# Kernel optimization log

Measured on AMD Instinct MI355X. Metric: run time of the kernel, lower is better.

Reference implementation:

```python
import jax, jax.numpy as jnp
import numpy as np

# ---- static config (from init_kwargs) ----
B, H, W, C = 4, 256, 256, 96
WS, SS, NH = 8, 4, 3            # window_size, shift_size, num_heads
N = WS * WS                     # tokens per window = 64
NW = (H // WS) * (W // WS)      # windows per image = 1024
HD = C // NH                    # head_dim = 32
SCALE = HD ** -0.5
MLP_H = int(C * 4.0)
EPS = 1e-5


def _relative_position_index():
    coords = np.stack(np.meshgrid(np.arange(WS), np.arange(WS), indexing='ij'))  # (2, WS, WS)
    cf = coords.reshape(2, -1)                       # (2, N)
    rel = (cf[:, :, None] - cf[:, None, :]).transpose(1, 2, 0).astype(np.int64)  # (N, N, 2)
    rel[:, :, 0] += WS - 1
    rel[:, :, 1] += WS - 1
    rel[:, :, 0] *= 2 * WS - 1
    return rel.sum(-1)                               # (N, N) in [0, (2WS-1)^2)


def _attn_mask():
    img = np.zeros((H, W))
    cnt = 0
    slices = (slice(0, -WS), slice(-WS, -SS), slice(-SS, None))
    for hs in slices:
        for ws in slices:
            img[hs, ws] = cnt
            cnt += 1
    m = img.reshape(H // WS, WS, W // WS, WS).transpose(0, 2, 1, 3).reshape(-1, N)  # (NW, N)
    am = m[:, None, :] - m[:, :, None]               # (NW, N, N)
    return np.where(am != 0, -100.0, 0.0).astype(np.float32)


def setup_inputs() -> dict:
    key = jax.random.key(0)
    ks = jax.random.split(key, 8)
    std = 0.02
    inp = {
        'x': jax.random.normal(ks[0], (B, H * W, C), jnp.float32),
        'g1': jnp.ones((C,), jnp.float32),
        'b1': jnp.zeros((C,), jnp.float32),
        'qkv_w': jax.random.normal(ks[1], (3 * C, C), jnp.float32) * std,
        'qkv_b': jnp.zeros((3 * C,), jnp.float32),
        'rpb_table': jax.random.normal(ks[2], ((2 * WS - 1) ** 2, NH), jnp.float32) * std,
        'proj_w': jax.random.normal(ks[3], (C, C), jnp.float32) * std,
        'proj_b': jnp.zeros((C,), jnp.float32),
        'g2': jnp.ones((C,), jnp.float32),
        'b2': jnp.zeros((C,), jnp.float32),
        'fc1_w': jax.random.normal(ks[4], (MLP_H, C), jnp.float32) * std,
        'fc1_b': jnp.zeros((MLP_H,), jnp.float32),
        'fc2_w': jax.random.normal(ks[5], (C, MLP_H), jnp.float32) * std,
        'fc2_b': jnp.zeros((C,), jnp.float32),
        'attn_mask': jnp.asarray(_attn_mask()),
        'rel_index': jnp.asarray(_relative_position_index(), jnp.int32),
    }
    return inp


def _ln(x, g, b):
    mu = jnp.mean(x, -1, keepdims=True)
    var = jnp.mean(jnp.square(x - mu), -1, keepdims=True)
    return (x - mu) * jax.lax.rsqrt(var + EPS) * g + b


def reference(x, g1, b1, qkv_w, qkv_b, rpb_table, proj_w, proj_b,
              g2, b2, fc1_w, fc1_b, fc2_w, fc2_b, attn_mask, rel_index):
    shortcut = x
    h = _ln(x, g1, b1).reshape(B, H, W, C)
    # cyclic shift
    h = jnp.roll(h, (-SS, -SS), axis=(1, 2))
    # window partition -> (B*NW, N, C)
    xw = h.reshape(B, H // WS, WS, W // WS, WS, C).transpose(0, 1, 3, 2, 4, 5).reshape(-1, N, C)
    # qkv projection
    qkv = (xw @ qkv_w.T + qkv_b).reshape(-1, N, 3, NH, HD).transpose(2, 0, 3, 1, 4)  # (3, B_, NH, N, HD)
    q, k, v = qkv[0] * SCALE, qkv[1], qkv[2]
    attn = jnp.einsum('bhnd,bhmd->bhnm', q, k)       # (B_, NH, N, N)
    # gathered relative position bias: (N, N, NH) -> (NH, N, N)
    bias = rpb_table[rel_index].transpose(2, 0, 1)
    attn = attn + bias[None]
    # shifted-window mask
    attn = attn.reshape(B, NW, NH, N, N) + attn_mask[None, :, None]
    attn = jax.nn.softmax(attn.reshape(-1, NH, N, N), axis=-1)
    o = jnp.einsum('bhnm,bhmd->bhnd', attn, v).transpose(0, 2, 1, 3).reshape(-1, N, C)
    o = o @ proj_w.T + proj_b
    # window reverse + reverse shift
    o = o.reshape(B, H // WS, W // WS, WS, WS, C).transpose(0, 1, 3, 2, 4, 5).reshape(B, H, W, C)
    o = jnp.roll(o, (SS, SS), axis=(1, 2)).reshape(B, H * W, C)
    x = shortcut + o
    h2 = _ln(x, g2, b2)
    h2 = jax.nn.gelu(h2 @ fc1_w.T + fc1_b, approximate=False) @ fc2_w.T + fc2_b
    return x + h2
```

## Files before the change

kernel.cpp:

```cpp
#include <hip/hip_runtime.h>
#include <hip/hip_bf16.h>
#include <math.h>

constexpr float SCALE_ = 0.17677669529663687f;

typedef float f32x4 __attribute__((ext_vector_type(4)));
typedef short bf16x8 __attribute__((ext_vector_type(8)));
typedef short short4v __attribute__((ext_vector_type(4)));
#define MFMA __builtin_amdgcn_mfma_f32_16x16x32_bf16


__device__ inline short f2bf(float f) {
    __hip_bfloat16 h = __float2bfloat16(f);
    return *reinterpret_cast<short*>(&h);
}
__device__ inline float bf2f(short s) {
    union { unsigned u; float f; } v; v.u = ((unsigned)(unsigned short)s) << 16;
    return v.f;
}
__device__ inline float gelu_erf(float v) {
    float z  = v * 0.70710678f;
    float z2 = fminf(z * z, 1.5f);
    float p  =      0.00012055333f;
    p = p * z2 -    0.00085483270f;
    p = p * z2 +    0.0052239776f;
    p = p * z2 -    0.0268661706f;
    p = p * z2 +    0.1128379167f;
    p = p * z2 -    0.3761263890f;
    p = p * z2 +    1.1283791671f;
    float er = z * p;
    float t  = 0.5f * v;
    return t * er + t;
}

__global__ __launch_bounds__(256)
void prep_weights(const float* __restrict__ qkv_w, const float* __restrict__ proj_w,
                  const float* __restrict__ fc1_w, const float* __restrict__ fc2_w,
                  short* __restrict__ ws)
{
    int i = blockIdx.x * 256 + threadIdx.x;
    if (i >= 110592) return;
    float v;
    if      (i < 27648)  v = qkv_w[i];
    else if (i < 36864)  v = proj_w[i - 27648];
    else if (i < 73728)  v = fc1_w[i - 36864];
    else                 v = fc2_w[i - 73728];
    ws[i] = f2bf(v);
}

__global__ __launch_bounds__(256)
void prep_comb(const float* __restrict__ rpb, const int* __restrict__ rel,
               const float* __restrict__ mask, short* __restrict__ comb)
{
    int e = blockIdx.x * 256 + threadIdx.x;
    if (e >= 49152) return;
    int t   = e / 12288;
    int rem = e - t * 12288;
    int h   = rem >> 12;
    int ij  = rem & 4095;
    const int rep[4] = {0, 31, 992, 1023};
    comb[e] = f2bf(rpb[rel[ij] * 3 + h] + mask[(long)rep[t] * 4096 + ij]);
}

__global__ __launch_bounds__(256, 3)
void attn_kernel(const float* __restrict__ x,
                 const float* __restrict__ g1, const float* __restrict__ b1,
                 const short* __restrict__ qkv_wb, const float* __restrict__ qkv_b,
                 const short* __restrict__ proj_wb, const float* __restrict__ proj_b,
                 const short* __restrict__ comb,
                 float* __restrict__ xnew)
{
    __shared__ short aL[64][104];
    __shared__ short qpL[64][104];
    __shared__ short kL[64][104];
    __shared__ short vT[96][72];

    const int tid  = threadIdx.x;
    const int wave = tid >> 6, lane = tid & 63;
    const int lr = lane & 15, lg = lane >> 4;
    const int blk = blockIdx.x;
    const int b = blk >> 10, wi = blk & 1023;
    const int wh = wi >> 5, ww = wi & 31;
    const int mtyp = ((wh == 31) ? 2 : 0) + ((ww == 31) ? 1 : 0);

    auto tok_of = [&](int n) -> int {
        int r = n >> 3, c = n & 7;
        int gh = (wh * 8 + r + 4) & 255;
        int gw = (ww * 8 + c + 4) & 255;
        return b * 65536 + gh * 256 + gw;
    };

    {
        const int n = tid >> 2, s = tid & 3;
        const float* xr = x + (long)tok_of(n) * 96 + s * 24;
        float xv[24];
        #pragma unroll
        for (int i = 0; i < 6; i++) {
            float4 t = ((const float4*)xr)[i];
            xv[4*i]=t.x; xv[4*i+1]=t.y; xv[4*i+2]=t.z; xv[4*i+3]=t.w;
        }
        float s1 = 0.f, s2 = 0.f;
        #pragma unroll
        for (int i = 0; i < 24; i++) { s1 += xv[i]; s2 += xv[i]*xv[i]; }
        s1 += __shfl_xor(s1, 1); s2 += __shfl_xor(s2, 1);
        s1 += __shfl_xor(s1, 2); s2 += __shfl_xor(s2, 2);
        float mu = s1 * (1.0f/96.0f);
        float var = s2 * (1.0f/96.0f) - mu*mu;
        float rs = rsqrtf(var + 1e-5f);
        #pragma unroll
        for (int c = 0; c < 24; c++)
            aL[n][s*24+c] = f2bf((xv[c]-mu)*rs*g1[s*24+c] + b1[s*24+c]);
    }
    __syncthreads();

    {
        const int wm = wave >> 1, wn = wave & 1;
        bf16x8 afr[2][3];
        #pragma unroll
        for (int mt = 0; mt < 2; mt++)
            #pragma unroll
            for (int kt = 0; kt < 3; kt++)
                afr[mt][kt] = *(const bf16x8*)&aL[(2*wm+mt)*16 + lr][kt*32 + lg*8];
        for (int nt0 = 0; nt0 < 9; nt0++) {
            const int nt = wn * 9 + nt0;
            const int o  = nt * 16 + lr;
            bf16x8 bfr[3];
            #pragma unroll
            for (int kt = 0; kt < 3; kt++)
                bfr[kt] = *(const bf16x8*)&qkv_wb[(long)o * 96 + kt*32 + lg*8];
            const float bias = qkv_b[o];
            #pragma unroll
            for (int mt = 0; mt < 2; mt++) {
                f32x4 acc = {bias, bias, bias, bias};
                #pragma unroll
                for (int kt = 0; kt < 3; kt++)
                    acc = MFMA(afr[mt][kt], bfr[kt], acc, 0, 0, 0);
                const int row0 = (2*wm+mt)*16 + lg*4;
                if (nt < 6) {
                    #pragma unroll
                    for (int r = 0; r < 4; r++) qpL[row0+r][o] = f2bf(acc[r]*SCALE_);
                } else if (nt < 12) {
                    #pragma unroll
                    for (int r = 0; r < 4; r++) kL[row0+r][o-96] = f2bf(acc[r]);
                } else {
                    #pragma unroll
                    for (int r = 0; r < 4; r++) vT[o-192][row0+r] = f2bf(acc[r]);
                }
            }
        }
    }
    __syncthreads();

    bf16x8 qf[3];
    #pragma unroll
    for (int h = 0; h < 3; h++)
        qf[h] = *(const bf16x8*)&qpL[wave*16 + lr][h*32 + lg*8];

    for (int h = 0; h < 3; h++) {
        const short* cb = comb + (mtyp * 3 + h) * 4096;
        float sv[4][4];
        #pragma unroll
        for (int nt = 0; nt < 4; nt++) {
            bf16x8 kf = *(const bf16x8*)&kL[nt*16 + lr][h*32 + lg*8];
            f32x4 s = MFMA(qf[h], kf, (f32x4){0.f,0.f,0.f,0.f}, 0, 0, 0);
            #pragma unroll
            for (int r = 0; r < 4; r++) {
                int i = wave*16 + lg*4 + r;
                int j = nt*16 + lr;
                sv[nt][r] = s[r] + bf2f(cb[i*64 + j]);
            }
        }
        float mx[4], sm[4];
        #pragma unroll
        for (int r = 0; r < 4; r++) {
            mx[r] = fmaxf(fmaxf(sv[0][r], sv[1][r]), fmaxf(sv[2][r], sv[3][r]));
            mx[r] = fmaxf(mx[r], __shfl_xor(mx[r], 1));
            mx[r] = fmaxf(mx[r], __shfl_xor(mx[r], 2));
            mx[r] = fmaxf(mx[r], __shfl_xor(mx[r], 4));
            mx[r] = fmaxf(mx[r], __shfl_xor(mx[r], 8));
            sm[r] = 0.f;
        }
        #pragma unroll
        for (int nt = 0; nt < 4; nt++)
            #pragma unroll
            for (int r = 0; r < 4; r++) { sv[nt][r] = __expf(sv[nt][r]-mx[r]); sm[r] += sv[nt][r]; }
        #pragma unroll
        for (int r = 0; r < 4; r++) {
            sm[r] += __shfl_xor(sm[r], 1);
            sm[r] += __shfl_xor(sm[r], 2);
            sm[r] += __shfl_xor(sm[r], 4);
            sm[r] += __shfl_xor(sm[r], 8);
            sm[r] = 1.0f / sm[r];
        }
        #pragma unroll
        for (int nt = 0; nt < 4; nt++)
            #pragma unroll
            for (int r = 0; r < 4; r++)
                qpL[wave*16 + lg*4 + r][nt*16 + lr] = f2bf(sv[nt][r]*sm[r]);

        bf16x8 pf[2];
        #pragma unroll
        for (int kt = 0; kt < 2; kt++)
            pf[kt] = *(const bf16x8*)&qpL[wave*16 + lr][kt*32 + lg*8];
        #pragma unroll
        for (int nt = 0; nt < 2; nt++) {
            f32x4 acc = {0.f,0.f,0.f,0.f};
            #pragma unroll
            for (int kt = 0; kt < 2; kt++) {
                bf16x8 vf = *(const bf16x8*)&vT[h*32 + nt*16 + lr][kt*32 + lg*8];
                acc = MFMA(pf[kt], vf, acc, 0, 0, 0);
            }
            #pragma unroll
            for (int r = 0; r < 4; r++)
                aL[wave*16 + lg*4 + r][h*32 + nt*16 + lr] = f2bf(acc[r]);
        }
    }
    __syncthreads();

    {
        const int wm = wave >> 1, wn = wave & 1;
        bf16x8 afr[2][3];
        #pragma unroll
        for (int mt = 0; mt < 2; mt++)
            #pragma unroll
            for (int kt = 0; kt < 3; kt++)
                afr[mt][kt] = *(const bf16x8*)&aL[(2*wm+mt)*16 + lr][kt*32 + lg*8];
        for (int nt0 = 0; nt0 < 3; nt0++) {
            const int nt = wn * 3 + nt0;
            const int c  = nt * 16 + lr;
            bf16x8 bfr[3];
            #pragma unroll
            for (int kt = 0; kt < 3; kt++)
                bfr[kt] = *(const bf16x8*)&proj_wb[(long)c * 96 + kt*32 + lg*8];
            const float bias = proj_b[c];
            #pragma unroll
            for (int mt = 0; mt < 2; mt++) {
                f32x4 acc = {bias, bias, bias, bias};
                #pragma unroll
                for (int kt = 0; kt < 3; kt++)
                    acc = MFMA(afr[mt][kt], bfr[kt], acc, 0, 0, 0);
                #pragma unroll
                for (int r = 0; r < 4; r++) {
                    int i = (2*wm+mt)*16 + lg*4 + r;
                    long ad = (long)tok_of(i) * 96 + c;
                    xnew[ad] = acc[r] + x[ad];
                }
            }
        }
    }
}

__global__ __launch_bounds__(256, 4)
void mlp_kernel(const float* __restrict__ g2, const float* __restrict__ b2,
                const short* __restrict__ fc1_wb, const float* __restrict__ fc1_b,
                const short* __restrict__ fc2_wb, const float* __restrict__ fc2_b,
                float* __restrict__ xio)
{
    __shared__ short smem[4 * 3328];
    const int tid  = threadIdx.x;
    const int wave = tid >> 6, lane = tid & 63;
    const int lr = lane & 15, lg = lane >> 4;
    short* wl = smem + wave * 3328;
    const long tok0 = (long)blockIdx.x * 128 + wave * 32;
    const long base = tok0 * 96;

    #pragma unroll
    for (int p = 0; p < 2; p++) {
        const int tl = p*16 + (lane >> 2);
        const int s  = lane & 3;
        const float* xr = xio + base + (long)tl * 96 + s * 24;
        float xv[24];
        #pragma unroll
        for (int i = 0; i < 6; i++) {
            float4 t = ((const float4*)xr)[i];
            xv[4*i]=t.x; xv[4*i+1]=t.y; xv[4*i+2]=t.z; xv[4*i+3]=t.w;
        }
        float s1 = 0.f, s2 = 0.f;
        #pragma unroll
        for (int i = 0; i < 24; i++) { s1 += xv[i]; s2 += xv[i]*xv[i]; }
        s1 += __shfl_xor(s1, 1); s2 += __shfl_xor(s2, 1);
        s1 += __shfl_xor(s1, 2); s2 += __shfl_xor(s2, 2);
        float mu  = s1 * (1.0f/96.0f);
        float var = s2 * (1.0f/96.0f) - mu*mu;
        float rs  = rsqrtf(var + 1e-5f);
        #pragma unroll
        for (int j = 0; j < 12; j++) {
            const int ch = s*24 + 2*j;
            unsigned lo = (unsigned short)f2bf((xv[2*j  ]-mu)*rs*g2[ch  ] + b2[ch  ]);
            unsigned hi = (unsigned short)f2bf((xv[2*j+1]-mu)*rs*g2[ch+1] + b2[ch+1]);
            *(unsigned*)&wl[tl*104 + ch] = lo | (hi << 16);
        }
    }
    bf16x8 bx[2][3];
    #pragma unroll
    for (int tt = 0; tt < 2; tt++)
        #pragma unroll
        for (int kt = 0; kt < 3; kt++)
            bx[tt][kt] = *(const bf16x8*)&wl[(tt*16+lr)*104 + kt*32 + lg*8];
    asm volatile("s_waitcnt lgkmcnt(0)" ::: "memory");

    f32x4 facc[2][6];
    #pragma unroll
    for (int nt = 0; nt < 6; nt++) {
        const float4 bb = *(const float4*)&fc2_b[nt*16 + lg*4];
        facc[0][nt] = (f32x4){bb.x, bb.y, bb.z, bb.w};
        facc[1][nt] = facc[0][nt];
    }

    for (int c = 0; c < 6; c++) {
        #pragma unroll
        for (int ss = 0; ss < 2; ss++) {
            f32x4 a1[2][2];
            #pragma unroll
            for (int h2 = 0; h2 < 2; h2++) {
                const int ht = ss*2 + h2;
                const int o  = c*64 + ht*16 + lr;
                bf16x8 wfr[3];
                #pragma unroll
                for (int kt = 0; kt < 3; kt++)
                    wfr[kt] = *(const bf16x8*)&fc1_wb[(long)o * 96 + kt*32 + lg*8];
                const float4 bi = *(const float4*)&fc1_b[c*64 + ht*16 + lg*4];
                const f32x4 binit = {bi.x, bi.y, bi.z, bi.w};
                #pragma unroll
                for (int tt = 0; tt < 2; tt++) {
                    f32x4 acc = binit;
                    #pragma unroll
                    for (int kt = 0; kt < 3; kt++)
                        acc = MFMA(wfr[kt], bx[tt][kt], acc, 0, 0, 0);
                    a1[h2][tt] = acc;
                }
            }
            #pragma unroll
            for (int h2 = 0; h2 < 2; h2++)
                #pragma unroll
                for (int tt = 0; tt < 2; tt++) {
                    short4v sv;
                    #pragma unroll
                    for (int r = 0; r < 4; r++)
                        sv[r] = f2bf(gelu_erf(a1[h2][tt][r]));
                    const int tok = tt*16 + lr;
                    const int hid = (ss*2 + h2)*16 + lg*4;
                    *(short4v*)&wl[tok*72 + hid] = sv;
                }
        }
        asm volatile("" ::: "memory");
        #pragma unroll
        for (int tt = 0; tt < 2; tt++) {
            bf16x8 hf[2];
            #pragma unroll
            for (int kt = 0; kt < 2; kt++)
                hf[kt] = *(const bf16x8*)&wl[(tt*16+lr)*72 + kt*32 + lg*8];
            #pragma unroll
            for (int nt = 0; nt < 6; nt++) {
                #pragma unroll
                for (int kt = 0; kt < 2; kt++) {
                    bf16x8 wf2 = *(const bf16x8*)&fc2_wb[(long)(nt*16+lr)*384 + c*64 + kt*32 + lg*8];
                    facc[tt][nt] = MFMA(wf2, hf[kt], facc[tt][nt], 0, 0, 0);
                }
            }
        }
        asm volatile("" ::: "memory");
    }

    #pragma unroll
    for (int tt = 0; tt < 2; tt++)
        #pragma unroll
        for (int nt = 0; nt < 6; nt++) {
            const long ad = base + (long)(tt*16 + lr) * 96 + nt*16 + lg*4;
            float4 o = *(const float4*)&xio[ad];
            o.x += facc[tt][nt][0]; o.y += facc[tt][nt][1];
            o.z += facc[tt][nt][2]; o.w += facc[tt][nt][3];
            *(float4*)&xio[ad] = o;
        }
}

extern "C" void kernel_launch(void* const* d_in, const int* in_sizes, int n_in,
                              void* d_out, int out_size, void* d_ws, size_t ws_size,
                              hipStream_t stream)
{
    const float* x      = (const float*)d_in[0];
    const float* g1     = (const float*)d_in[1];
    const float* b1     = (const float*)d_in[2];
    const float* qkv_w  = (const float*)d_in[3];
    const float* qkv_b  = (const float*)d_in[4];
    const float* rpb    = (const float*)d_in[5];
    const float* proj_w = (const float*)d_in[6];
    const float* proj_b = (const float*)d_in[7];
    const float* g2     = (const float*)d_in[8];
    const float* b2     = (const float*)d_in[9];
    const float* fc1_w  = (const float*)d_in[10];
    const float* fc1_b  = (const float*)d_in[11];
    const float* fc2_w  = (const float*)d_in[12];
    const float* fc2_b  = (const float*)d_in[13];
    const float* mask   = (const float*)d_in[14];
    const int*   rel    = (const int*)d_in[15];
    float* out = (float*)d_out;

    short* wsS    = (short*)d_ws;
    short* qkv_wb = wsS;
    short* proj_wb= wsS + 27648;
    short* fc1_wb = wsS + 36864;
    short* fc2_wb = wsS + 73728;
    short* comb   = wsS + 110592;

    prep_weights<<<432, 256, 0, stream>>>(qkv_w, proj_w, fc1_w, fc2_w, wsS);
    prep_comb<<<192, 256, 0, stream>>>(rpb, rel, mask, comb);
    attn_kernel<<<4096, 256, 0, stream>>>(x, g1, b1, qkv_wb, qkv_b,
                                          proj_wb, proj_b, comb, out);
    mlp_kernel<<<2048, 256, 0, stream>>>(g2, b2, fc1_wb, fc1_b, fc2_wb, fc2_b, out);
}
```

Baseline: 277.3 us.

## Split MLP tile across waves in 2x2 grid with shared hidden buffer

Before, each wave ran the full MLP on its own 32 tokens, so every wave streamed all fc1/fc2 weight rows. Now a 256-thread block handles 64 tokens, and its four waves form a 2x2 grid. Each wave computes half the hidden units for half the tokens in fc1, and half the output columns in fc2. The GELU hidden chunk goes to double-buffered shared memory and is shared across waves, which halves per-wave weight-fragment loads. The cost is block-wide __syncthreads each chunk and a doubled grid size.

```diff
diff --git a/kernel.cpp b/kernel.cpp
--- a/kernel.cpp
+++ b/kernel.cpp
@@ -256,19 +256,19 @@
                 const short* __restrict__ fc2_wb, const float* __restrict__ fc2_b,
                 float* __restrict__ xio)
 {
-    __shared__ short smem[4 * 3328];
+    __shared__ short smem[9216];
+    short (*aL)[104]    = (short(*)[104])smem;
+    short (*hch)[64][72] = (short(*)[64][72])smem;
+
     const int tid  = threadIdx.x;
     const int wave = tid >> 6, lane = tid & 63;
     const int lr = lane & 15, lg = lane >> 4;
-    short* wl = smem + wave * 3328;
-    const long tok0 = (long)blockIdx.x * 128 + wave * 32;
-    const long base = tok0 * 96;
-
-    #pragma unroll
-    for (int p = 0; p < 2; p++) {
-        const int tl = p*16 + (lane >> 2);
-        const int s  = lane & 3;
-        const float* xr = xio + base + (long)tl * 96 + s * 24;
+    const int wm = wave >> 1, wn = wave & 1;
+    const long base = (long)blockIdx.x * 6144;
+
+    {
+        const int n = tid >> 2, s = tid & 3;
+        const float* xr = xio + base + n * 96 + s * 24;
         float xv[24];
         #pragma unroll
         for (int i = 0; i < 6; i++) {
@@ -288,88 +288,89 @@
             const int ch = s*24 + 2*j;
             unsigned lo = (unsigned short)f2bf((xv[2*j  ]-mu)*rs*g2[ch  ] + b2[ch  ]);
             unsigned hi = (unsigned short)f2bf((xv[2*j+1]-mu)*rs*g2[ch+1] + b2[ch+1]);
-            *(unsigned*)&wl[tl*104 + ch] = lo | (hi << 16);
-        }
-    }
+            *(unsigned*)&aL[n][ch] = lo | (hi << 16);
+        }
+    }
+    __syncthreads();
+
     bf16x8 bx[2][3];
     #pragma unroll
     for (int tt = 0; tt < 2; tt++)
         #pragma unroll
         for (int kt = 0; kt < 3; kt++)
-            bx[tt][kt] = *(const bf16x8*)&wl[(tt*16+lr)*104 + kt*32 + lg*8];
-    asm volatile("s_waitcnt lgkmcnt(0)" ::: "memory");
-
-    f32x4 facc[2][6];
+            bx[tt][kt] = *(const bf16x8*)&aL[(wn*2+tt)*16 + lr][kt*32 + lg*8];
+    __syncthreads();
+
+    f32x4 facc[3][2];
     #pragma unroll
-    for (int nt = 0; nt < 6; nt++) {
-        const float4 bb = *(const float4*)&fc2_b[nt*16 + lg*4];
-        facc[0][nt] = (f32x4){bb.x, bb.y, bb.z, bb.w};
-        facc[1][nt] = facc[0][nt];
+    for (int nt = 0; nt < 3; nt++) {
+        const float4 bb = *(const float4*)&fc2_b[(wm*3+nt)*16 + lg*4];
+        facc[nt][0] = (f32x4){bb.x, bb.y, bb.z, bb.w};
+        facc[nt][1] = facc[nt][0];
     }
 
     for (int c = 0; c < 6; c++) {
-        #pragma unroll
-        for (int ss = 0; ss < 2; ss++) {
-            f32x4 a1[2][2];
-            #pragma unroll
-            for (int h2 = 0; h2 < 2; h2++) {
-                const int ht = ss*2 + h2;
-                const int o  = c*64 + ht*16 + lr;
-                bf16x8 wfr[3];
+        const int cbuf = c & 1;
+        f32x4 acc1[2][2];
+        #pragma unroll
+        for (int h2 = 0; h2 < 2; h2++) {
+            const int ht = wm*2 + h2;
+            const int o  = c*64 + ht*16 + lr;
+            bf16x8 wfr[3];
+            #pragma unroll
+            for (int kt = 0; kt < 3; kt++)
+                wfr[kt] = *(const bf16x8*)&fc1_wb[(long)o * 96 + kt*32 + lg*8];
+            const float4 bi = *(const float4*)&fc1_b[c*64 + ht*16 + lg*4];
+            const f32x4 binit = {bi.x, bi.y, bi.z, bi.w};
+            #pragma unroll
+            for (int tt = 0; tt < 2; tt++) {
+                f32x4 acc = binit;
                 #pragma unroll
                 for (int kt = 0; kt < 3; kt++)
-                    wfr[kt] = *(const bf16x8*)&fc1_wb[(long)o * 96 + kt*32 + lg*8];
-                const float4 bi = *(const float4*)&fc1_b[c*64 + ht*16 + lg*4];
-                const f32x4 binit = {bi.x, bi.y, bi.z, bi.w};
-                #pragma unroll
-                for (int tt = 0; tt < 2; tt++) {
-                    f32x4 acc = binit;
-                    #pragma unroll
-                    for (int kt = 0; kt < 3; kt++)
-                        acc = MFMA(wfr[kt], bx[tt][kt], acc, 0, 0, 0);
-                    a1[h2][tt] = acc;
-                }
-            }
-            #pragma unroll
-            for (int h2 = 0; h2 < 2; h2++)
-                #pragma unroll
-                for (int tt = 0; tt < 2; tt++) {
-                    short4v sv;
-                    #pragma unroll
-                    for (int r = 0; r < 4; r++)
-                        sv[r] = f2bf(gelu_erf(a1[h2][tt][r]));
-                    const int tok = tt*16 + lr;
-                    const int hid = (ss*2 + h2)*16 + lg*4;
-                    *(short4v*)&wl[tok*72 + hid] = sv;
-                }
-        }
-        asm volatile("" ::: "memory");
+                    acc = MFMA(wfr[kt], bx[tt][kt], acc, 0, 0, 0);
+                acc1[h2][tt] = acc;
+            }
+        }
+        #pragma unroll
+        for (int h2 = 0; h2 < 2; h2++)
+            #pragma unroll
+            for (int tt = 0; tt < 2; tt++) {
+                short4v sv;
+                #pragma unroll
+                for (int r = 0; r < 4; r++)
+                    sv[r] = f2bf(gelu_erf(acc1[h2][tt][r]));
+                const int tok = (wn*2+tt)*16 + lr;
+                const int hid = (wm*2+h2)*16 + lg*4;
+                *(short4v*)&hch[cbuf][tok][hid] = sv;
+            }
+        __syncthreads();
         #pragma unroll
         for (int tt = 0; tt < 2; tt++) {
             bf16x8 hf[2];
             #pragma unroll
             for (int kt = 0; kt < 2; kt++)
-                hf[kt] = *(const bf16x8*)&wl[(tt*16+lr)*72 + kt*32 + lg*8];
-            #pragma unroll
-            for (int nt = 0; nt < 6; nt++) {
+                hf[kt] = *(const bf16x8*)&hch[cbuf][(wn*2+tt)*16 + lr][kt*32 + lg*8];
+            #pragma unroll
+            for (int nt = 0; nt < 3; nt++) {
                 #pragma unroll
                 for (int kt = 0; kt < 2; kt++) {
-                    bf16x8 wf2 = *(const bf16x8*)&fc2_wb[(long)(nt*16+lr)*384 + c*64 + kt*32 + lg*8];
-                    facc[tt][nt] = MFMA(wf2, hf[kt], facc[tt][nt], 0, 0, 0);
+                    bf16x8 wf2 = *(const bf16x8*)&fc2_wb[(long)((wm*3+nt)*16 + lr) * 384 + c*64 + kt*32 + lg*8];
+                    facc[nt][tt] = MFMA(wf2, hf[kt], facc[nt][tt], 0, 0, 0);
                 }
             }
         }
-        asm volatile("" ::: "memory");
     }
 
     #pragma unroll
-    for (int tt = 0; tt < 2; tt++)
-        #pragma unroll
-        for (int nt = 0; nt < 6; nt++) {
-            const long ad = base + (long)(tt*16 + lr) * 96 + nt*16 + lg*4;
+    for (int nt = 0; nt < 3; nt++)
+        #pragma unroll
+        for (int tt = 0; tt < 2; tt++) {
+            const int tok  = (wn*2+tt)*16 + lr;
+            const int ocol = (wm*3+nt)*16 + lg*4;
+            const long ad  = base + (long)tok * 96 + ocol;
             float4 o = *(const float4*)&xio[ad];
-            o.x += facc[tt][nt][0]; o.y += facc[tt][nt][1];
-            o.z += facc[tt][nt][2]; o.w += facc[tt][nt][3];
+            o.x += facc[nt][tt][0]; o.y += facc[nt][tt][1];
+            o.z += facc[nt][tt][2]; o.w += facc[nt][tt][3];
             *(float4*)&xio[ad] = o;
         }
 }
@@ -407,5 +408,5 @@
     prep_comb<<<192, 256, 0, stream>>>(rpb, rel, mask, comb);
     attn_kernel<<<4096, 256, 0, stream>>>(x, g1, b1, qkv_wb, qkv_b,
                                           proj_wb, proj_b, comb, out);
-    mlp_kernel<<<2048, 256, 0, stream>>>(g2, b2, fc1_wb, fc1_b, fc2_wb, fc2_b, out);
-}
+    mlp_kernel<<<4096, 256, 0, stream>>>(g2, b2, fc1_wb, fc1_b, fc2_wb, fc2_b, out);
+}
```

Measured after the change: 240.0 us. -13.4%, faster.
